# Kernel optimization log

Hardware: AMD Instinct MI355X
Metric: run time of the kernel (lower is better)

The kernel has to match this reference:

```python
import jax, jax.numpy as jnp
import numpy as np

E, N, F = 50000, 25000, 32

def setup_inputs() -> dict:
    key = jax.random.key(0)
    ks = jax.random.split(key, 8)
    efeat = jax.random.normal(ks[0], (E, F), dtype=jnp.float32) * 0.2
    initial_efeats = jax.random.normal(ks[1], (E, F), dtype=jnp.float32) * 0.2
    # msg_fn / attn_fn: Linear(F, F*F)
    Wm = jax.random.normal(ks[2], (F * F, F), dtype=jnp.float32) * 0.05
    bm = jnp.zeros((F * F,), dtype=jnp.float32)
    Wa = jax.random.normal(ks[3], (F * F, F), dtype=jnp.float32) * 0.05
    ba = jnp.zeros((F * F,), dtype=jnp.float32)
    src = jax.random.randint(ks[4], (E,), 0, N, dtype=jnp.int32)
    dst = jax.random.randint(ks[5], (E,), 0, N, dtype=jnp.int32)
    return {"efeat": efeat, "initial_efeats": initial_efeats, "Wm": Wm, "bm": bm,
            "Wa": Wa, "ba": ba, "src": src, "dst": dst, "num_nodes": N}

def reference(efeat, initial_efeats, Wm, bm, Wa, ba, src, dst, num_nodes):
    e, f = efeat.shape
    # edge-conditioned transform matrices: [E, F, F]
    w_m = (efeat @ Wm.T + bm).reshape(e, f, f)
    w_a = (efeat @ Wa.T + ba).reshape(e, f, f)
    h = efeat[:, :, None]                 # [E, F, 1]
    ih = initial_efeats[:, :, None]       # [E, F, 1]
    e1 = w_m * h                          # [E, F, F]
    exp_e2 = jnp.exp(w_a * h)             # [E, F, F]
    initial_e1 = w_m * ih
    exp_initial_e2 = jnp.exp(w_a * ih)
    # scatter-sum exp weights to destination nodes, gather back at src
    sum_exp_node = jax.ops.segment_sum(exp_e2, dst, num_segments=num_nodes)  # [N, F, F]
    sum_exp = sum_exp_node[src] - exp_e2 + exp_initial_e2
    h1 = exp_e2 * e1
    initial_h1 = exp_initial_e2 * initial_e1
    m_node = jax.ops.segment_sum(h1, dst, num_segments=num_nodes)            # [N, F, F]
    h2 = (m_node[src] - h1 + initial_h1) / sum_exp
    return h2.sum(axis=1)                 # [E, F]
```

## Files before the change

kernel.cpp:

```cpp
#include <hip/hip_runtime.h>
#include <hip/hip_fp16.h>
#include <math.h>
#include <stdint.h>


#define FDIM   32
#define NNODES 25000

typedef __attribute__((ext_vector_type(8))) short bf16x8;
typedef __attribute__((ext_vector_type(4))) float f32x4;
typedef __attribute__((ext_vector_type(8))) unsigned short us8;

__device__ __forceinline__ unsigned short f2bf(float f) {
    unsigned u = __float_as_uint(f);
    return (unsigned short)((u + 0x7FFFu + ((u >> 16) & 1u)) >> 16);
}
__device__ __forceinline__ unsigned short pack_e5(float am, float aa) {
    auto hp = __builtin_amdgcn_cvt_pkrtz(am, aa);
    unsigned u;
    __builtin_memcpy(&u, &hp, 4);
    return (unsigned short)__builtin_amdgcn_perm(0u, u, 0x0301u);
}
__device__ __forceinline__ void dec2(unsigned v, float& am, float& aa) {
    am = __half2float(__ushort_as_half((unsigned short)((v & 0xFFu) << 8)));
    aa = __half2float(__ushort_as_half((unsigned short)(v & 0xFF00u)));
}

__global__ __launch_bounds__(256) void zero_f4(float4* __restrict__ p, int n4) {
    int i = blockIdx.x * blockDim.x + threadIdx.x;
    int stride = gridDim.x * blockDim.x;
    float4 z = make_float4(0.f, 0.f, 0.f, 0.f);
    for (; i < n4; i += stride) p[i] = z;
}

__global__ __launch_bounds__(256) void k_hist(
    const int* __restrict__ src, const int* __restrict__ dst,
    int* __restrict__ cnt_src, int* __restrict__ cnt_dst, int E) {
    int e = blockIdx.x * blockDim.x + threadIdx.x;
    if (e < E) {
        atomicAdd(&cnt_dst[dst[e]], 1);
        atomicAdd(&cnt_src[src[e]], 1);
    }
}

__global__ __launch_bounds__(256) void k_scan2_prep(
    const int* __restrict__ cnt_dst, int* __restrict__ off_dst, int* __restrict__ cur_dst,
    const int* __restrict__ cnt_src, int* __restrict__ off_src, int* __restrict__ cur_src,
    int n,
    const float* __restrict__ Wm, const float* __restrict__ Wa,
    short* __restrict__ wbuf)
{
    if (blockIdx.x >= 2) {
        int idx = (blockIdx.x - 2) * blockDim.x + threadIdx.x;
        if (idx >= 2 * 64 * 64) return;
        int mat  = idx >> 12;
        int jt   = (idx >> 6) & 63;
        int lane = idx & 63;
        const float* W = mat ? Wa : Wm;
        const float* s = W + (size_t)(jt * 16 + (lane & 15)) * FDIM + (lane >> 4) * 8;
        bf16x8 v;
#pragma unroll
        for (int t = 0; t < 8; ++t) v[t] = (short)f2bf(s[t]);
        *(bf16x8*)(wbuf + (size_t)idx * 8) = v;
        return;
    }
    const int* cnt = blockIdx.x ? cnt_src : cnt_dst;
    int* off = blockIdx.x ? off_src : off_dst;
    int* cur = blockIdx.x ? cur_src : cur_dst;
    __shared__ int wsum[4];
    __shared__ int carry_sh;
    const int tid = threadIdx.x, lane = tid & 63, w = tid >> 6;
    if (tid == 0) carry_sh = 0;
    __syncthreads();
    for (int base = 0; base < n; base += 1024) {
        int i0 = base + tid * 4;
        int v0 = (i0 + 0 < n) ? cnt[i0 + 0] : 0;
        int v1 = (i0 + 1 < n) ? cnt[i0 + 1] : 0;
        int v2 = (i0 + 2 < n) ? cnt[i0 + 2] : 0;
        int v3 = (i0 + 3 < n) ? cnt[i0 + 3] : 0;
        int s = v0 + v1 + v2 + v3;
        int inc = s;
        for (int d = 1; d < 64; d <<= 1) {
            int t = __shfl_up(inc, d, 64);
            if (lane >= d) inc += t;
        }
        if (lane == 63) wsum[w] = inc;
        __syncthreads();
        int wbase = 0;
        for (int k = 0; k < w; ++k) wbase += wsum[k];
        int carry = carry_sh;
        int excl = carry + wbase + inc - s;
        if (i0 + 0 < n) { off[i0 + 0] = excl; cur[i0 + 0] = excl; } excl += v0;
        if (i0 + 1 < n) { off[i0 + 1] = excl; cur[i0 + 1] = excl; } excl += v1;
        if (i0 + 2 < n) { off[i0 + 2] = excl; cur[i0 + 2] = excl; } excl += v2;
        if (i0 + 3 < n) { off[i0 + 3] = excl; cur[i0 + 3] = excl; }
        __syncthreads();
        if (tid == 255) carry_sh = carry + wbase + inc;
    }
    __syncthreads();
    if (tid == 0) off[n] = carry_sh;
}

__global__ __launch_bounds__(256) void k_scatter(
    const int* __restrict__ src, const int* __restrict__ dst,
    int* __restrict__ cur_src, int* __restrict__ cur_dst,
    int* __restrict__ eb_src, int* __restrict__ eb_dst, int E) {
    int e = blockIdx.x * blockDim.x + threadIdx.x;
    if (e < E) {
        int p = atomicAdd(&cur_dst[dst[e]], 1); eb_dst[p] = e;
        int q = atomicAdd(&cur_src[src[e]], 1); eb_src[q] = e;
    }
}

__global__ __launch_bounds__(256) void gemm(
    const float* __restrict__ efeat,
    const float* __restrict__ bm, const float* __restrict__ ba,
    const short* __restrict__ wbuf,
    unsigned short* __restrict__ buf, int E)
{
    const int lane = threadIdx.x & 63;
    const int wid  = threadIdx.x >> 6;
    const int et   = blockIdx.x * 4 + wid;
    if (et * 16 >= E) return;
    const int r16 = lane & 15;
    const int kq  = lane >> 4;

    const float* xa = efeat + (size_t)(et * 16 + r16) * FDIM + kq * 8;
    bf16x8 afrag;
#pragma unroll
    for (int t = 0; t < 8; ++t) afrag[t] = (short)f2bf(xa[t]);

    for (int jt = 0; jt < 64; ++jt) {
        bf16x8 bfm = *(const bf16x8*)(wbuf + ((size_t)(jt)      * 64 + lane) * 8);
        bf16x8 bfa = *(const bf16x8*)(wbuf + ((size_t)(64 + jt) * 64 + lane) * 8);
        const int j = jt * 16 + r16;
        const float biasm = bm[j], biasa = ba[j];
        f32x4 accm = {biasm, biasm, biasm, biasm};
        f32x4 acca = {biasa, biasa, biasa, biasa};
        accm = __builtin_amdgcn_mfma_f32_16x16x32_bf16(afrag, bfm, accm, 0, 0, 0);
        acca = __builtin_amdgcn_mfma_f32_16x16x32_bf16(afrag, bfa, acca, 0, 0, 0);
#pragma unroll
        for (int r = 0; r < 4; ++r) {
            int e = et * 16 + kq * 4 + r;
            buf[(size_t)e * 1024 + j] = pack_e5(accm[r], acca[r]);
        }
    }
}

__global__ __launch_bounds__(256) void consume(
    const float* __restrict__ efeat, const float* __restrict__ ifeat,
    const unsigned short* __restrict__ buf,
    const int* __restrict__ off_dst, const int* __restrict__ eb_dst,
    const int* __restrict__ off_src, const int* __restrict__ eb_src,
    float* __restrict__ out)
{
    const int l  = threadIdx.x & 63;
    const int w  = threadIdx.x >> 6;
    const int n  = blockIdx.x * 4 + w;
    if (n >= NNODES) return;
    const int ih = l >> 2;

    float S[16], M[16];
#pragma unroll
    for (int t = 0; t < 16; ++t) { S[t] = 0.f; M[t] = 0.f; }

    const int a0 = off_dst[n], a1 = off_dst[n + 1];
    for (int idx = a0; idx < a1; ++idx) {
        int e = __builtin_amdgcn_readfirstlane(eb_dst[idx]);
#pragma unroll
        for (int qq = 0; qq < 2; ++qq) {
            us8 pv = *(const us8*)(buf + (size_t)e * 1024 + qq * 512 + l * 8);
            float xi = efeat[e * FDIM + qq * 16 + ih];
#pragma unroll
            for (int t = 0; t < 8; ++t) {
                float am, aa; dec2(pv[t], am, aa);
                float e2 = __expf(aa * xi);
                S[qq * 8 + t] += e2;
                M[qq * 8 + t] = fmaf(e2, am * xi, M[qq * 8 + t]);
            }
        }
    }

    const int b0 = off_src[n], b1 = off_src[n + 1];
    for (int idx = b0; idx < b1; ++idx) {
        int e = __builtin_amdgcn_readfirstlane(eb_src[idx]);
        float acc[8];
#pragma unroll
        for (int t = 0; t < 8; ++t) acc[t] = 0.f;
#pragma unroll
        for (int qq = 0; qq < 2; ++qq) {
            us8 pv = *(const us8*)(buf + (size_t)e * 1024 + qq * 512 + l * 8);
            float xi  = efeat[e * FDIM + qq * 16 + ih];
            float x0i = ifeat[e * FDIM + qq * 16 + ih];
#pragma unroll
            for (int t = 0; t < 8; ++t) {
                float am, aa; dec2(pv[t], am, aa);
                float e2  = __expf(aa * xi);
                float h1  = e2 * (am * xi);
                float ei2 = __expf(aa * x0i);
                float ih1 = ei2 * (am * x0i);
                float den = (S[qq * 8 + t] - e2) + ei2;
                float num = (M[qq * 8 + t] - h1) + ih1;
                float h2  = num * __builtin_amdgcn_rcpf(den);
                if (!isfinite(h2)) h2 = 0.f;
                acc[t] += h2;
            }
        }
#pragma unroll
        for (int t = 0; t < 8; ++t) {
            acc[t] += __shfl_xor(acc[t], 4, 64);
            acc[t] += __shfl_xor(acc[t], 8, 64);
            acc[t] += __shfl_xor(acc[t], 16, 64);
            acc[t] += __shfl_xor(acc[t], 32, 64);
        }
        if (l < 4) {
            float* op = out + (size_t)e * FDIM + l * 8;
            *(float4*)op       = make_float4(acc[0], acc[1], acc[2], acc[3]);
            *(float4*)(op + 4) = make_float4(acc[4], acc[5], acc[6], acc[7]);
        }
    }
}

extern "C" void kernel_launch(void* const* d_in, const int* in_sizes, int n_in,
                              void* d_out, int out_size, void* d_ws, size_t ws_size,
                              hipStream_t stream) {
    const float* efeat = (const float*)d_in[0];
    const float* ifeat = (const float*)d_in[1];
    const float* Wm    = (const float*)d_in[2];
    const float* bm    = (const float*)d_in[3];
    const float* Wa    = (const float*)d_in[4];
    const float* ba    = (const float*)d_in[5];
    const int*   src   = (const int*)d_in[6];
    const int*   dst   = (const int*)d_in[7];
    const int E = in_sizes[6];
    const int N = NNODES;
    float* out = (float*)d_out;

    int* cnt_dst = (int*)d_ws;
    int* cnt_src = cnt_dst + N;
    int* off_dst = cnt_src + N;
    int* off_src = off_dst + (N + 1);
    int* cur_dst = off_src + (N + 1);
    int* cur_src = cur_dst + N;
    int* eb_dst  = cur_src + N;
    int* eb_src  = eb_dst + E;
    short* wbuf  = (short*)(((uintptr_t)(eb_src + E) + 255) & ~(uintptr_t)255);
    unsigned short* buf =
        (unsigned short*)(((uintptr_t)(wbuf + 2 * 64 * 64 * 8) + 255) & ~(uintptr_t)255);

    zero_f4<<<64, 256, 0, stream>>>((float4*)cnt_dst, (2 * N) / 4);
    k_hist<<<(E + 255) / 256, 256, 0, stream>>>(src, dst, cnt_src, cnt_dst, E);
    k_scan2_prep<<<34, 256, 0, stream>>>(cnt_dst, off_dst, cur_dst,
                                         cnt_src, off_src, cur_src, N,
                                         Wm, Wa, wbuf);
    k_scatter<<<(E + 255) / 256, 256, 0, stream>>>(src, dst, cur_src, cur_dst,
                                                   eb_src, eb_dst, E);

    const int etiles = (E + 15) / 16;
    gemm<<<(etiles + 3) / 4, 256, 0, stream>>>(efeat, bm, ba, wbuf, buf, E);
    consume<<<(N + 3) / 4, 256, 0, stream>>>(efeat, ifeat, buf,
                                             off_dst, eb_dst,
                                             off_src, eb_src, out);
}
```

Measured before the change: 222.1 us.

## Split consume into per-node reduction and per-edge output kernels with fp16 SM buffer

The single node-centric consume kernel is replaced by two kernels. The first reduces S and M per destination node and stores them as packed fp16 pairs in a node buffer. The second processes one edge per wave, gathering the node's S/M by src, which removes the src CSR build (histogram, scan, scatter) and balances work across edges. The GEMM is also transposed so each lane writes contiguous packed 8-byte chunks with vectorized bias loads. In exchange, the node buffer adds about 100MB of extra traffic, and storing S/M in fp16 risks overflow or precision loss.

```diff
diff --git a/kernel.cpp b/kernel.cpp
--- a/kernel.cpp
+++ b/kernel.cpp
@@ -25,6 +25,16 @@
     am = __half2float(__ushort_as_half((unsigned short)((v & 0xFFu) << 8)));
     aa = __half2float(__ushort_as_half((unsigned short)(v & 0xFF00u)));
 }
+__device__ __forceinline__ unsigned pack_sm(float S, float M) {
+    auto hp = __builtin_amdgcn_cvt_pkrtz(S, M);
+    unsigned u;
+    __builtin_memcpy(&u, &hp, 4);
+    return u;
+}
+__device__ __forceinline__ void unpack_sm(unsigned v, float& S, float& M) {
+    S = __half2float(__ushort_as_half((unsigned short)(v & 0xFFFFu)));
+    M = __half2float(__ushort_as_half((unsigned short)(v >> 16)));
+}
 
 __global__ __launch_bounds__(256) void zero_f4(float4* __restrict__ p, int n4) {
     int i = blockIdx.x * blockDim.x + threadIdx.x;
@@ -34,24 +44,19 @@
 }
 
 __global__ __launch_bounds__(256) void k_hist(
-    const int* __restrict__ src, const int* __restrict__ dst,
-    int* __restrict__ cnt_src, int* __restrict__ cnt_dst, int E) {
+    const int* __restrict__ dst, int* __restrict__ cnt_dst, int E) {
     int e = blockIdx.x * blockDim.x + threadIdx.x;
-    if (e < E) {
-        atomicAdd(&cnt_dst[dst[e]], 1);
-        atomicAdd(&cnt_src[src[e]], 1);
-    }
-}
-
-__global__ __launch_bounds__(256) void k_scan2_prep(
+    if (e < E) atomicAdd(&cnt_dst[dst[e]], 1);
+}
+
+__global__ __launch_bounds__(256) void k_scan_prep(
     const int* __restrict__ cnt_dst, int* __restrict__ off_dst, int* __restrict__ cur_dst,
-    const int* __restrict__ cnt_src, int* __restrict__ off_src, int* __restrict__ cur_src,
     int n,
     const float* __restrict__ Wm, const float* __restrict__ Wa,
     short* __restrict__ wbuf)
 {
-    if (blockIdx.x >= 2) {
-        int idx = (blockIdx.x - 2) * blockDim.x + threadIdx.x;
+    if (blockIdx.x >= 1) {
+        int idx = (blockIdx.x - 1) * blockDim.x + threadIdx.x;
         if (idx >= 2 * 64 * 64) return;
         int mat  = idx >> 12;
         int jt   = (idx >> 6) & 63;
@@ -64,9 +69,9 @@
         *(bf16x8*)(wbuf + (size_t)idx * 8) = v;
         return;
     }
-    const int* cnt = blockIdx.x ? cnt_src : cnt_dst;
-    int* off = blockIdx.x ? off_src : off_dst;
-    int* cur = blockIdx.x ? cur_src : cur_dst;
+    const int* cnt = cnt_dst;
+    int* off = off_dst;
+    int* cur = cur_dst;
     __shared__ int wsum[4];
     __shared__ int carry_sh;
     const int tid = threadIdx.x, lane = tid & 63, w = tid >> 6;
@@ -102,13 +107,12 @@
 }
 
 __global__ __launch_bounds__(256) void k_scatter(
-    const int* __restrict__ src, const int* __restrict__ dst,
-    int* __restrict__ cur_src, int* __restrict__ cur_dst,
-    int* __restrict__ eb_src, int* __restrict__ eb_dst, int E) {
+    const int* __restrict__ dst, int* __restrict__ cur_dst,
+    int* __restrict__ eb_dst, int E) {
     int e = blockIdx.x * blockDim.x + threadIdx.x;
     if (e < E) {
-        int p = atomicAdd(&cur_dst[dst[e]], 1); eb_dst[p] = e;
-        int q = atomicAdd(&cur_src[src[e]], 1); eb_src[q] = e;
+        int p = atomicAdd(&cur_dst[dst[e]], 1);
+        eb_dst[p] = e;
     }
 }
 
@@ -122,41 +126,43 @@
     const int wid  = threadIdx.x >> 6;
     const int et   = blockIdx.x * 4 + wid;
     if (et * 16 >= E) return;
-    const int r16 = lane & 15;
-    const int kq  = lane >> 4;
-
-    const float* xa = efeat + (size_t)(et * 16 + r16) * FDIM + kq * 8;
-    bf16x8 afrag;
-#pragma unroll
-    for (int t = 0; t < 8; ++t) afrag[t] = (short)f2bf(xa[t]);
+    const int r16  = lane & 15;
+    const int quad = lane >> 4;
+
+    const float* xa = efeat + (size_t)(et * 16 + r16) * FDIM + quad * 8;
+    bf16x8 efrag;
+#pragma unroll
+    for (int t = 0; t < 8; ++t) efrag[t] = (short)f2bf(xa[t]);
+
+    unsigned short* brow = buf + (size_t)(et * 16 + r16) * 1024 + quad * 4;
 
     for (int jt = 0; jt < 64; ++jt) {
-        bf16x8 bfm = *(const bf16x8*)(wbuf + ((size_t)(jt)      * 64 + lane) * 8);
-        bf16x8 bfa = *(const bf16x8*)(wbuf + ((size_t)(64 + jt) * 64 + lane) * 8);
-        const int j = jt * 16 + r16;
-        const float biasm = bm[j], biasa = ba[j];
-        f32x4 accm = {biasm, biasm, biasm, biasm};
-        f32x4 acca = {biasa, biasa, biasa, biasa};
-        accm = __builtin_amdgcn_mfma_f32_16x16x32_bf16(afrag, bfm, accm, 0, 0, 0);
-        acca = __builtin_amdgcn_mfma_f32_16x16x32_bf16(afrag, bfa, acca, 0, 0, 0);
-#pragma unroll
-        for (int r = 0; r < 4; ++r) {
-            int e = et * 16 + kq * 4 + r;
-            buf[(size_t)e * 1024 + j] = pack_e5(accm[r], acca[r]);
-        }
-    }
-}
-
-__global__ __launch_bounds__(256) void consume(
-    const float* __restrict__ efeat, const float* __restrict__ ifeat,
+        bf16x8 wm = *(const bf16x8*)(wbuf + ((size_t)(jt)      * 64 + lane) * 8);
+        bf16x8 wa = *(const bf16x8*)(wbuf + ((size_t)(64 + jt) * 64 + lane) * 8);
+        float4 bmv = *(const float4*)(bm + jt * 16 + quad * 4);
+        float4 bav = *(const float4*)(ba + jt * 16 + quad * 4);
+        f32x4 accm = {bmv.x, bmv.y, bmv.z, bmv.w};
+        f32x4 acca = {bav.x, bav.y, bav.z, bav.w};
+        accm = __builtin_amdgcn_mfma_f32_16x16x32_bf16(wm, efrag, accm, 0, 0, 0);
+        acca = __builtin_amdgcn_mfma_f32_16x16x32_bf16(wa, efrag, acca, 0, 0, 0);
+        unsigned lo = (unsigned)pack_e5(accm[0], acca[0])
+                    | ((unsigned)pack_e5(accm[1], acca[1]) << 16);
+        unsigned hi = (unsigned)pack_e5(accm[2], acca[2])
+                    | ((unsigned)pack_e5(accm[3], acca[3]) << 16);
+        uint2 pk = {lo, hi};
+        *(uint2*)(brow + jt * 16) = pk;
+    }
+}
+
+__global__ __launch_bounds__(256) void consume1(
+    const float* __restrict__ efeat,
     const unsigned short* __restrict__ buf,
     const int* __restrict__ off_dst, const int* __restrict__ eb_dst,
-    const int* __restrict__ off_src, const int* __restrict__ eb_src,
-    float* __restrict__ out)
-{
-    const int l  = threadIdx.x & 63;
-    const int w  = threadIdx.x >> 6;
-    const int n  = blockIdx.x * 4 + w;
+    unsigned int* __restrict__ SMnode)
+{
+    const int l = threadIdx.x & 63;
+    const int w = threadIdx.x >> 6;
+    const int n = blockIdx.x * 4 + w;
     if (n >= NNODES) return;
     const int ih = l >> 2;
 
@@ -180,44 +186,72 @@
             }
         }
     }
-
-    const int b0 = off_src[n], b1 = off_src[n + 1];
-    for (int idx = b0; idx < b1; ++idx) {
-        int e = __builtin_amdgcn_readfirstlane(eb_src[idx]);
-        float acc[8];
-#pragma unroll
-        for (int t = 0; t < 8; ++t) acc[t] = 0.f;
-#pragma unroll
-        for (int qq = 0; qq < 2; ++qq) {
-            us8 pv = *(const us8*)(buf + (size_t)e * 1024 + qq * 512 + l * 8);
-            float xi  = efeat[e * FDIM + qq * 16 + ih];
-            float x0i = ifeat[e * FDIM + qq * 16 + ih];
-#pragma unroll
-            for (int t = 0; t < 8; ++t) {
-                float am, aa; dec2(pv[t], am, aa);
-                float e2  = __expf(aa * xi);
-                float h1  = e2 * (am * xi);
-                float ei2 = __expf(aa * x0i);
-                float ih1 = ei2 * (am * x0i);
-                float den = (S[qq * 8 + t] - e2) + ei2;
-                float num = (M[qq * 8 + t] - h1) + ih1;
-                float h2  = num * __builtin_amdgcn_rcpf(den);
-                if (!isfinite(h2)) h2 = 0.f;
-                acc[t] += h2;
-            }
+    unsigned int* row = SMnode + (size_t)n * 1024 + l * 8;
+#pragma unroll
+    for (int qq = 0; qq < 2; ++qq) {
+        uint4 d0, d1;
+        d0.x = pack_sm(S[qq*8+0], M[qq*8+0]); d0.y = pack_sm(S[qq*8+1], M[qq*8+1]);
+        d0.z = pack_sm(S[qq*8+2], M[qq*8+2]); d0.w = pack_sm(S[qq*8+3], M[qq*8+3]);
+        d1.x = pack_sm(S[qq*8+4], M[qq*8+4]); d1.y = pack_sm(S[qq*8+5], M[qq*8+5]);
+        d1.z = pack_sm(S[qq*8+6], M[qq*8+6]); d1.w = pack_sm(S[qq*8+7], M[qq*8+7]);
+        *(uint4*)(row + qq * 512)     = d0;
+        *(uint4*)(row + qq * 512 + 4) = d1;
+    }
+}
+
+__global__ __launch_bounds__(256) void consume2(
+    const float* __restrict__ efeat, const float* __restrict__ ifeat,
+    const unsigned short* __restrict__ buf,
+    const unsigned int* __restrict__ SMnode,
+    const int* __restrict__ src,
+    float* __restrict__ out, int E)
+{
+    const int l = threadIdx.x & 63;
+    const int w = threadIdx.x >> 6;
+    const int e = blockIdx.x * 4 + w;
+    if (e >= E) return;
+    const int ih = l >> 2;
+    const int s  = src[e];
+
+    float acc[8];
+#pragma unroll
+    for (int t = 0; t < 8; ++t) acc[t] = 0.f;
+
+#pragma unroll
+    for (int qq = 0; qq < 2; ++qq) {
+        us8 pv = *(const us8*)(buf + (size_t)e * 1024 + qq * 512 + l * 8);
+        const unsigned int* smrow = SMnode + (size_t)s * 1024 + qq * 512 + l * 8;
+        uint4 sm0 = *(const uint4*)(smrow);
+        uint4 sm1 = *(const uint4*)(smrow + 4);
+        float xi  = efeat[e * FDIM + qq * 16 + ih];
+        float x0i = ifeat[e * FDIM + qq * 16 + ih];
+        unsigned smv[8] = {sm0.x, sm0.y, sm0.z, sm0.w, sm1.x, sm1.y, sm1.z, sm1.w};
+#pragma unroll
+        for (int t = 0; t < 8; ++t) {
+            float S, M; unpack_sm(smv[t], S, M);
+            float am, aa; dec2(pv[t], am, aa);
+            float e2  = __expf(aa * xi);
+            float h1  = e2 * (am * xi);
+            float ei2 = __expf(aa * x0i);
+            float ih1 = ei2 * (am * x0i);
+            float den = (S - e2) + ei2;
+            float num = (M - h1) + ih1;
+            float h2  = num * __builtin_amdgcn_rcpf(den);
+            if (!isfinite(h2)) h2 = 0.f;
+            acc[t] += h2;
         }
-#pragma unroll
-        for (int t = 0; t < 8; ++t) {
-            acc[t] += __shfl_xor(acc[t], 4, 64);
-            acc[t] += __shfl_xor(acc[t], 8, 64);
-            acc[t] += __shfl_xor(acc[t], 16, 64);
-            acc[t] += __shfl_xor(acc[t], 32, 64);
-        }
-        if (l < 4) {
-            float* op = out + (size_t)e * FDIM + l * 8;
-            *(float4*)op       = make_float4(acc[0], acc[1], acc[2], acc[3]);
-            *(float4*)(op + 4) = make_float4(acc[4], acc[5], acc[6], acc[7]);
-        }
+    }
+#pragma unroll
+    for (int t = 0; t < 8; ++t) {
+        acc[t] += __shfl_xor(acc[t], 4, 64);
+        acc[t] += __shfl_xor(acc[t], 8, 64);
+        acc[t] += __shfl_xor(acc[t], 16, 64);
+        acc[t] += __shfl_xor(acc[t], 32, 64);
+    }
+    if (l < 4) {
+        float* op = out + (size_t)e * FDIM + l * 8;
+        *(float4*)op       = make_float4(acc[0], acc[1], acc[2], acc[3]);
+        *(float4*)(op + 4) = make_float4(acc[4], acc[5], acc[6], acc[7]);
     }
 }
 
@@ -237,28 +271,25 @@
     float* out = (float*)d_out;
 
     int* cnt_dst = (int*)d_ws;
-    int* cnt_src = cnt_dst + N;
-    int* off_dst = cnt_src + N;
-    int* off_src = off_dst + (N + 1);
-    int* cur_dst = off_src + (N + 1);
-    int* cur_src = cur_dst + N;
-    int* eb_dst  = cur_src + N;
-    int* eb_src  = eb_dst + E;
-    short* wbuf  = (short*)(((uintptr_t)(eb_src + E) + 255) & ~(uintptr_t)255);
+    int* off_dst = cnt_dst + N;
+    int* cur_dst = off_dst + (N + 1);
+    int* eb_dst  = cur_dst + N;
+    short* wbuf  = (short*)(((uintptr_t)(eb_dst + E) + 255) & ~(uintptr_t)255);
     unsigned short* buf =
         (unsigned short*)(((uintptr_t)(wbuf + 2 * 64 * 64 * 8) + 255) & ~(uintptr_t)255);
-
-    zero_f4<<<64, 256, 0, stream>>>((float4*)cnt_dst, (2 * N) / 4);
-    k_hist<<<(E + 255) / 256, 256, 0, stream>>>(src, dst, cnt_src, cnt_dst, E);
-    k_scan2_prep<<<34, 256, 0, stream>>>(cnt_dst, off_dst, cur_dst,
-                                         cnt_src, off_src, cur_src, N,
-                                         Wm, Wa, wbuf);
-    k_scatter<<<(E + 255) / 256, 256, 0, stream>>>(src, dst, cur_src, cur_dst,
-                                                   eb_src, eb_dst, E);
+    unsigned int* SMnode =
+        (unsigned int*)(buf + (size_t)E * 1024);
+
+    zero_f4<<<25, 256, 0, stream>>>((float4*)cnt_dst, N / 4);
+    k_hist<<<(E + 255) / 256, 256, 0, stream>>>(dst, cnt_dst, E);
+    k_scan_prep<<<33, 256, 0, stream>>>(cnt_dst, off_dst, cur_dst, N,
+                                        Wm, Wa, wbuf);
+    k_scatter<<<(E + 255) / 256, 256, 0, stream>>>(dst, cur_dst, eb_dst, E);
 
     const int etiles = (E + 15) / 16;
     gemm<<<(etiles + 3) / 4, 256, 0, stream>>>(efeat, bm, ba, wbuf, buf, E);
-    consume<<<(N + 3) / 4, 256, 0, stream>>>(efeat, ifeat, buf,
-                                             off_dst, eb_dst,
-                                             off_src, eb_src, out);
-}
+    consume1<<<(N + 3) / 4, 256, 0, stream>>>(efeat, buf, off_dst, eb_dst,
+                                              SMnode);
+    consume2<<<(E + 3) / 4, 256, 0, stream>>>(efeat, ifeat, buf, SMnode, src,
+                                              out, E);
+}
```

After: 254.6 us. 14.6% more time.
